# Performance work log

Hardware: AMD Instinct MI355X
Metric: run time of the kernel (lower is better)

## Reference

```python
import jax, jax.numpy as jnp
import numpy as np

N = 50000   # nodes
E = 800000  # edges
G = 64      # graphs
D_IN = 128
D_OUT = 64
HID = 2 * D_OUT  # 128, hidden width of non-final layers
EPS = 1e-5


def _seg_sum(v, idx, n):
    return jax.ops.segment_sum(v, idx, num_segments=n)


def _gcn(x, W, b, src, dst, n):
    # GCNConv with default add_self_loops=True, edge_weight=1, sym norm
    xw = x @ W                                            # [N, out]
    deg = _seg_sum(jnp.ones(src.shape[0], x.dtype), dst, n) + 1.0  # +1 self loop
    dis = jax.lax.rsqrt(deg)                              # deg^{-1/2}, deg>=1
    norm = dis[src] * dis[dst]                            # [E]
    agg = _seg_sum(norm[:, None] * xw[src], dst, n)       # gather-scale-scatter
    return agg + (dis * dis)[:, None] * xw + b            # self-loop term + bias


def _mpnn_layer(x, src, dst, edge_attr, gw, gb, ew, eb, n):
    h = _gcn(x, gw, gb, src, dst, n)
    e = jax.nn.relu(edge_attr[:, None] * ew + eb)         # Linear(1,out).relu per edge
    msg = h[src] + e                                      # message = x_j + edge_attr
    cnt = _seg_sum(jnp.ones(src.shape[0], x.dtype), dst, n)
    return _seg_sum(msg, dst, n) / jnp.clip(cnt, 1.0)[:, None]  # scatter-mean


def _ln(x, g, b):
    # node-wise LayerNorm over feature dim
    mu = x.mean(-1, keepdims=True)
    var = x.var(-1, keepdims=True)
    return (x - mu) * jax.lax.rsqrt(var + EPS) * g + b


def setup_inputs() -> dict:
    key = jax.random.key(0)
    ks = jax.random.split(key, 24)
    x = jax.random.normal(ks[0], (N, D_IN), jnp.float32)
    edge_index = jax.random.randint(ks[1], (2, E), 0, N, dtype=jnp.int64)
    edge_attr = jax.random.uniform(ks[2], (E,), jnp.float32)
    batch = jnp.sort(jax.random.randint(ks[3], (N,), 0, G, dtype=jnp.int64))

    def lin(k, fan_in, shape):
        return jax.random.uniform(k, shape, jnp.float32, -1.0, 1.0) / np.sqrt(fan_in)

    # layer 0: in 128 -> 128; layer 1: 128 -> 128; layer 2: 128 -> 64
    inp = {
        "x": x, "edge_index": edge_index, "edge_attr": edge_attr, "batch": batch,
        "gcn_w0": lin(ks[4], D_IN, (D_IN, HID)),  "gcn_b0": jnp.zeros((HID,), jnp.float32),
        "edge_w0": lin(ks[5], 1, (HID,)),          "edge_b0": lin(ks[6], 1, (HID,)),
        "ln_g0": jnp.ones((HID,), jnp.float32),   "ln_b0": jnp.zeros((HID,), jnp.float32),
        "gcn_w1": lin(ks[7], HID, (HID, HID)),    "gcn_b1": jnp.zeros((HID,), jnp.float32),
        "edge_w1": lin(ks[8], 1, (HID,)),          "edge_b1": lin(ks[9], 1, (HID,)),
        "ln_g1": jnp.ones((HID,), jnp.float32),   "ln_b1": jnp.zeros((HID,), jnp.float32),
        "gcn_w2": lin(ks[10], HID, (HID, D_OUT)), "gcn_b2": jnp.zeros((D_OUT,), jnp.float32),
        "edge_w2": lin(ks[11], 1, (D_OUT,)),       "edge_b2": lin(ks[12], 1, (D_OUT,)),
    }
    return inp


def reference(x, edge_index, edge_attr, batch,
              gcn_w0, gcn_b0, edge_w0, edge_b0, ln_g0, ln_b0,
              gcn_w1, gcn_b1, edge_w1, edge_b1, ln_g1, ln_b1,
              gcn_w2, gcn_b2, edge_w2, edge_b2):
    src, dst = edge_index[0], edge_index[1]
    h = _mpnn_layer(x, src, dst, edge_attr, gcn_w0, gcn_b0, edge_w0, edge_b0, N)
    h = _ln(jax.nn.relu(h), ln_g0, ln_b0)
    h = _mpnn_layer(h, src, dst, edge_attr, gcn_w1, gcn_b1, edge_w1, edge_b1, N)
    h = _ln(jax.nn.relu(h), ln_g1, ln_b1)
    h = _mpnn_layer(h, src, dst, edge_attr, gcn_w2, gcn_b2, edge_w2, edge_b2, N)
    # global_mean_pool
    cnt = _seg_sum(jnp.ones((N,), h.dtype), batch, G)
    z_pooled = _seg_sum(h, batch, G) / jnp.clip(cnt, 1.0)[:, None]
    return h, z_pooled
```

## Files before the change

### kernel.cpp

```cpp
#include <hip/hip_runtime.h>

#define NN 50000
#define NE 800000
#define NG 64
#define HID 128
#define DOUT 64
#define LN_EPS 1e-5f
#define NBUK 391
#define BCAP 3072
#define EPB 8192

typedef unsigned int uint32;
typedef unsigned short ushort16;

__device__ inline ushort16 f2bf(float f) {
  uint32 u = __float_as_uint(f);
  u += 0x7fffu + ((u >> 16) & 1u);
  return (ushort16)(u >> 16);
}
__device__ inline uint32 pack2(float x, float y) {
  return (uint32)f2bf(x) | ((uint32)f2bf(y) << 16);
}
__device__ inline float bflo(uint32 p) { return __uint_as_float(p << 16); }
__device__ inline float bfhi(uint32 p) { return __uint_as_float(p & 0xffff0000u); }

__global__ __launch_bounds__(256) void k_zero_f(float* p, int n) {
  int i = blockIdx.x * 256 + threadIdx.x;
  if (i < n) p[i] = 0.f;
}

__global__ __launch_bounds__(256) void k_init_bcur(int* __restrict__ bcur) {
  int i = blockIdx.x * 256 + threadIdx.x;
  if (i < NBUK) bcur[i] = i * BCAP;
}

__global__ __launch_bounds__(1024) void k_bucket(const int* __restrict__ src,
                                                 const int* __restrict__ dst,
                                                 const float* __restrict__ ea,
                                                 int* __restrict__ bcur,
                                                 uint2* __restrict__ tmp, int e) {
  __shared__ int hist[NBUK], lbase[NBUK], lcur[NBUK];
  int t = threadIdx.x;
  for (int i = t; i < NBUK; i += 1024) {
    hist[i] = 0;
    lcur[i] = 0;
  }
  __syncthreads();
  int base_e = blockIdx.x * EPB;
  int dstv[EPB / 1024];
#pragma unroll
  for (int k = 0; k < EPB / 1024; k++) {
    int i = base_e + k * 1024 + t;
    int d = (i < e) ? dst[i] : -1;
    dstv[k] = d;
    if (d >= 0) atomicAdd(&hist[d >> 7], 1);
  }
  __syncthreads();
  for (int i = t; i < NBUK; i += 1024) {
    int c = hist[i];
    int b = 0;
    if (c > 0) b = atomicAdd(&bcur[i], c);
    lbase[i] = b;
  }
  __syncthreads();
#pragma unroll
  for (int k = 0; k < EPB / 1024; k++) {
    int i = base_e + k * 1024 + t;
    int d = dstv[k];
    if (d >= 0) {
      int b = d >> 7;
      int r = atomicAdd(&lcur[b], 1);
      int pos = lbase[b] + r;
      if (pos < (b + 1) * BCAP) {
        uint2 rec;
        rec.x = (uint32)(src[i] & 0xffff) | ((uint32)(d & 127) << 16);
        rec.y = __float_as_uint(ea[i]);
        tmp[pos] = rec;
      }
    }
  }
}

__global__ __launch_bounds__(512) void k_bscan(const int* __restrict__ bcur,
                                               int* __restrict__ bbase,
                                               int* __restrict__ rowptr) {
  __shared__ int s[512];
  int t = threadIdx.x;
  int v = 0;
  if (t < NBUK) {
    v = bcur[t] - t * BCAP;
    if (v > BCAP) v = BCAP;
  }
  s[t] = v;
  __syncthreads();
  for (int off = 1; off < 512; off <<= 1) {
    int x = (t >= off) ? s[t - off] : 0;
    __syncthreads();
    s[t] += x;
    __syncthreads();
  }
  if (t < NBUK) bbase[t] = s[t] - v;
  if (t == 511) {
    bbase[NBUK] = s[511];
    rowptr[NN] = s[511];
  }
}

__global__ __launch_bounds__(256) void k_bsort(const uint2* __restrict__ tmp,
                                               const int* __restrict__ bcur,
                                               const int* __restrict__ bbase,
                                               int* __restrict__ rowptr,
                                               int* __restrict__ csrc,
                                               float* __restrict__ cea,
                                               float* __restrict__ dis,
                                               float* __restrict__ invc) {
  int b = blockIdx.x;
  __shared__ int hist[128], excl[128], cur[128];
  int t = threadIdx.x;
  if (t < 128) {
    hist[t] = 0;
    cur[t] = 0;
  }
  __syncthreads();
  int cnt = bcur[b] - b * BCAP;
  if (cnt > BCAP) cnt = BCAP;
  int tb = b * BCAP;
  int ob = bbase[b];
  for (int i = t; i < cnt; i += 256) {
    uint2 r = tmp[tb + i];
    atomicAdd(&hist[(r.x >> 16) & 127], 1);
  }
  __syncthreads();
  int myDeg = (t < 128) ? hist[t] : 0;
  for (int off = 1; off < 128; off <<= 1) {
    int x = 0;
    if (t < 128 && t >= off) x = hist[t - off];
    __syncthreads();
    if (t < 128) hist[t] += x;
    __syncthreads();
  }
  if (t < 128) {
    excl[t] = hist[t] - myDeg;
    int node = (b << 7) + t;
    if (node < NN) {
      rowptr[node] = ob + excl[t];
      dis[node] = rsqrtf((float)(myDeg + 1));
      invc[node] = (myDeg > 0) ? 1.0f / (float)myDeg : 1.0f;
    }
  }
  __syncthreads();
  for (int i = t; i < cnt; i += 256) {
    uint2 r = tmp[tb + i];
    int o = (r.x >> 16) & 127;
    int p = atomicAdd(&cur[o], 1);
    int pos = ob + excl[o] + p;
    csrc[pos] = (int)(r.x & 0xffffu);
    cea[pos] = __uint_as_float(r.y);
  }
}

template <int FOUT, bool IN_BF, bool OUT_BF>
__global__ __launch_bounds__(256) void k_gemm(const void* __restrict__ Xv,
                                              const float* __restrict__ W,
                                              void* __restrict__ Yv, int n) {
  const int FI = 128;
  __shared__ __align__(16) float xs[32][FI];
  int t = threadIdx.x;
  int row0 = blockIdx.x * 32;
  if (IN_BF) {
    const ushort16* Xb = (const ushort16*)Xv;
    for (int i = t; i < 32 * 32; i += 256) {
      int r = i >> 5, c = i & 31;
      uint2 v = make_uint2(0u, 0u);
      if (row0 + r < n) v = ((const uint2*)(Xb + (size_t)(row0 + r) * FI))[c];
      float4 f = {bflo(v.x), bfhi(v.x), bflo(v.y), bfhi(v.y)};
      ((float4*)xs[r])[c] = f;
    }
  } else {
    const float* X = (const float*)Xv;
    for (int i = t; i < 32 * FI / 4; i += 256) {
      int r = i / (FI / 4);
      int c = i % (FI / 4);
      float4 v = make_float4(0.f, 0.f, 0.f, 0.f);
      if (row0 + r < n) v = ((const float4*)(X + (size_t)(row0 + r) * FI))[c];
      ((float4*)xs[r])[c] = v;
    }
  }
  __syncthreads();
  const int CG = FOUT / 4;
  const int RG = 256 / CG;
  const int RPT = 32 / RG;
  int cg = t % CG;
  int rg = t / CG;
  float acc[RPT][4];
#pragma unroll
  for (int r = 0; r < RPT; r++)
#pragma unroll
    for (int c = 0; c < 4; c++) acc[r][c] = 0.f;

#pragma unroll 2
  for (int k4 = 0; k4 < FI / 4; k4++) {
    float4 wv[4];
#pragma unroll
    for (int kk = 0; kk < 4; kk++)
      wv[kk] = ((const float4*)(W + (size_t)(4 * k4 + kk) * FOUT))[cg];
#pragma unroll
    for (int r = 0; r < RPT; r++) {
      float4 xv = ((const float4*)xs[rg * RPT + r])[k4];
      acc[r][0] += xv.x * wv[0].x + xv.y * wv[1].x + xv.z * wv[2].x + xv.w * wv[3].x;
      acc[r][1] += xv.x * wv[0].y + xv.y * wv[1].y + xv.z * wv[2].y + xv.w * wv[3].y;
      acc[r][2] += xv.x * wv[0].z + xv.y * wv[1].z + xv.z * wv[2].z + xv.w * wv[3].z;
      acc[r][3] += xv.x * wv[0].w + xv.y * wv[1].w + xv.z * wv[2].w + xv.w * wv[3].w;
    }
  }
#pragma unroll
  for (int r = 0; r < RPT; r++) {
    int row = row0 + rg * RPT + r;
    if (row < n) {
      if (OUT_BF) {
        uint2 o = {pack2(acc[r][0], acc[r][1]), pack2(acc[r][2], acc[r][3])};
        ((uint2*)((ushort16*)Yv + (size_t)row * FOUT))[cg] = o;
      } else {
        float4 o = {acc[r][0], acc[r][1], acc[r][2], acc[r][3]};
        ((float4*)((float*)Yv + (size_t)row * FOUT))[cg] = o;
      }
    }
  }
}

__global__ __launch_bounds__(256) void k_agg_bf(const uint32* __restrict__ XWb,
                                                const float* __restrict__ dis,
                                                const int* __restrict__ rowptr,
                                                const int* __restrict__ csrc,
                                                const float* __restrict__ bias,
                                                uint32* __restrict__ Hb, int n) {
  int lane = threadIdx.x & 63;
  int node = blockIdx.x * 4 + (threadIdx.x >> 6);
  if (node >= n) return;
  float dn = dis[node];
  int beg = rowptr[node], end = rowptr[node + 1];
  float ax = 0.f, ay = 0.f;
  int i = beg;
  for (; i + 4 <= end; i += 4) {
    int s0 = csrc[i], s1 = csrc[i + 1], s2 = csrc[i + 2], s3 = csrc[i + 3];
    float n0 = dn * dis[s0], n1 = dn * dis[s1], n2 = dn * dis[s2], n3 = dn * dis[s3];
    uint32 p0 = XWb[(size_t)s0 * 64 + lane];
    uint32 p1 = XWb[(size_t)s1 * 64 + lane];
    uint32 p2 = XWb[(size_t)s2 * 64 + lane];
    uint32 p3 = XWb[(size_t)s3 * 64 + lane];
    ax += n0 * bflo(p0) + n1 * bflo(p1) + n2 * bflo(p2) + n3 * bflo(p3);
    ay += n0 * bfhi(p0) + n1 * bfhi(p1) + n2 * bfhi(p2) + n3 * bfhi(p3);
  }
  for (; i < end; i++) {
    int s = csrc[i];
    float nr = dn * dis[s];
    uint32 p = XWb[(size_t)s * 64 + lane];
    ax += nr * bflo(p);
    ay += nr * bfhi(p);
  }
  uint32 ps = XWb[(size_t)node * 64 + lane];
  float2 bb = ((const float2*)bias)[lane];
  float d2 = dn * dn;
  float hx = ax + d2 * bflo(ps) + bb.x;
  float hy = ay + d2 * bfhi(ps) + bb.y;
  Hb[(size_t)node * 64 + lane] = pack2(hx, hy);
}

__global__ __launch_bounds__(256) void k_msg_bf(const uint32* __restrict__ Hb,
                                                const float* __restrict__ ew,
                                                const float* __restrict__ eb,
                                                const int* __restrict__ rowptr,
                                                const int* __restrict__ csrc,
                                                const float* __restrict__ cea,
                                                const float* __restrict__ invc,
                                                const float* __restrict__ lng,
                                                const float* __restrict__ lnb,
                                                uint32* __restrict__ OUTb, int n) {
  int lane = threadIdx.x & 63;
  int node = blockIdx.x * 4 + (threadIdx.x >> 6);
  if (node >= n) return;
  int beg = rowptr[node], end = rowptr[node + 1];
  float2 w = ((const float2*)ew)[lane];
  float2 b = ((const float2*)eb)[lane];
  float ax = 0.f, ay = 0.f;
  int i = beg;
  for (; i + 4 <= end; i += 4) {
    int s0 = csrc[i], s1 = csrc[i + 1], s2 = csrc[i + 2], s3 = csrc[i + 3];
    float a0 = cea[i], a1 = cea[i + 1], a2 = cea[i + 2], a3 = cea[i + 3];
    uint32 p0 = Hb[(size_t)s0 * 64 + lane];
    uint32 p1 = Hb[(size_t)s1 * 64 + lane];
    uint32 p2 = Hb[(size_t)s2 * 64 + lane];
    uint32 p3 = Hb[(size_t)s3 * 64 + lane];
    ax += bflo(p0) + fmaxf(a0 * w.x + b.x, 0.f) + bflo(p1) + fmaxf(a1 * w.x + b.x, 0.f) +
          bflo(p2) + fmaxf(a2 * w.x + b.x, 0.f) + bflo(p3) + fmaxf(a3 * w.x + b.x, 0.f);
    ay += bfhi(p0) + fmaxf(a0 * w.y + b.y, 0.f) + bfhi(p1) + fmaxf(a1 * w.y + b.y, 0.f) +
          bfhi(p2) + fmaxf(a2 * w.y + b.y, 0.f) + bfhi(p3) + fmaxf(a3 * w.y + b.y, 0.f);
  }
  for (; i < end; i++) {
    int s = csrc[i];
    float a = cea[i];
    uint32 p = Hb[(size_t)s * 64 + lane];
    ax += bflo(p) + fmaxf(a * w.x + b.x, 0.f);
    ay += bfhi(p) + fmaxf(a * w.y + b.y, 0.f);
  }
  float ic = invc[node];
  float ox = fmaxf(ax * ic, 0.f);
  float oy = fmaxf(ay * ic, 0.f);
  float s1 = ox + oy;
  float s2 = ox * ox + oy * oy;
  for (int off = 32; off; off >>= 1) {
    s1 += __shfl_xor(s1, off, 64);
    s2 += __shfl_xor(s2, off, 64);
  }
  float mu = s1 * (1.f / 128.f);
  float var = s2 * (1.f / 128.f) - mu * mu;
  float r = rsqrtf(var + LN_EPS);
  float2 g = ((const float2*)lng)[lane];
  float2 bb = ((const float2*)lnb)[lane];
  ox = (ox - mu) * r * g.x + bb.x;
  oy = (oy - mu) * r * g.y + bb.y;
  OUTb[(size_t)node * 64 + lane] = pack2(ox, oy);
}

__global__ __launch_bounds__(256) void k_agg64(const float* __restrict__ XW,
                                               const float* __restrict__ dis,
                                               const int* __restrict__ rowptr,
                                               const int* __restrict__ csrc,
                                               const float* __restrict__ bias,
                                               float* __restrict__ H, int n) {
  int lane = threadIdx.x & 63;
  int node = blockIdx.x * 4 + (threadIdx.x >> 6);
  if (node >= n) return;
  float dn = dis[node];
  int beg = rowptr[node], end = rowptr[node + 1];
  float acc = 0.f;
  int i = beg;
  for (; i + 4 <= end; i += 4) {
    int s0 = csrc[i], s1 = csrc[i + 1], s2 = csrc[i + 2], s3 = csrc[i + 3];
    float n0 = dn * dis[s0], n1 = dn * dis[s1], n2 = dn * dis[s2], n3 = dn * dis[s3];
    acc += n0 * XW[(size_t)s0 * 64 + lane] + n1 * XW[(size_t)s1 * 64 + lane] +
           n2 * XW[(size_t)s2 * 64 + lane] + n3 * XW[(size_t)s3 * 64 + lane];
  }
  for (; i < end; i++) {
    int s = csrc[i];
    acc += dn * dis[s] * XW[(size_t)s * 64 + lane];
  }
  float d2 = dn * dn;
  H[(size_t)node * 64 + lane] = acc + d2 * XW[(size_t)node * 64 + lane] + bias[lane];
}

__global__ __launch_bounds__(256) void k_msg64(const float* __restrict__ H,
                                               const float* __restrict__ ew,
                                               const float* __restrict__ eb,
                                               const int* __restrict__ rowptr,
                                               const int* __restrict__ csrc,
                                               const float* __restrict__ cea,
                                               const float* __restrict__ invc,
                                               float* __restrict__ OUT, int n) {
  int lane = threadIdx.x & 63;
  int node = blockIdx.x * 4 + (threadIdx.x >> 6);
  if (node >= n) return;
  int beg = rowptr[node], end = rowptr[node + 1];
  float w = ew[lane], b = eb[lane];
  float acc = 0.f;
  int i = beg;
  for (; i + 4 <= end; i += 4) {
    int s0 = csrc[i], s1 = csrc[i + 1], s2 = csrc[i + 2], s3 = csrc[i + 3];
    float a0 = cea[i], a1 = cea[i + 1], a2 = cea[i + 2], a3 = cea[i + 3];
    acc += H[(size_t)s0 * 64 + lane] + fmaxf(a0 * w + b, 0.f) +
           H[(size_t)s1 * 64 + lane] + fmaxf(a1 * w + b, 0.f) +
           H[(size_t)s2 * 64 + lane] + fmaxf(a2 * w + b, 0.f) +
           H[(size_t)s3 * 64 + lane] + fmaxf(a3 * w + b, 0.f);
  }
  for (; i < end; i++) {
    int s = csrc[i];
    acc += H[(size_t)s * 64 + lane] + fmaxf(cea[i] * w + b, 0.f);
  }
  OUT[(size_t)node * 64 + lane] = acc * invc[node];
}

#define POOL_BLOCKS 256
__global__ __launch_bounds__(256) void k_pool_partial(const float* __restrict__ H,
                                                      const int* __restrict__ batch,
                                                      float* __restrict__ Z, int n) {
  int lane = threadIdx.x & 63;
  int wid = blockIdx.x * 4 + (threadIdx.x >> 6);
  const int WAVES = POOL_BLOCKS * 4;
  int per = (n + WAVES - 1) / WAVES;
  int beg = wid * per;
  int end = beg + per;
  if (end > n) end = n;
  if (beg >= end) return;
  int g = batch[beg];
  float acc = 0.f;
  for (int i = beg; i < end; i++) {
    int gi = batch[i];
    if (gi != g) {
      atomicAdd(&Z[g * 64 + lane], acc);
      acc = 0.f;
      g = gi;
    }
    acc += H[(size_t)i * 64 + lane];
  }
  atomicAdd(&Z[g * 64 + lane], acc);
}

__global__ __launch_bounds__(64) void k_pool_div(float* __restrict__ Z,
                                                 const int* __restrict__ batch, int n) {
  int g = blockIdx.x;
  __shared__ int scnt;
  if (threadIdx.x == 0) {
    int lo = 0, hi = n;
    while (lo < hi) { int m = (lo + hi) >> 1; if (batch[m] < g) lo = m + 1; else hi = m; }
    int b0 = lo;
    lo = 0; hi = n;
    while (lo < hi) { int m = (lo + hi) >> 1; if (batch[m] < g + 1) lo = m + 1; else hi = m; }
    scnt = lo - b0;
  }
  __syncthreads();
  float c = (float)scnt;
  if (c < 1.f) c = 1.f;
  Z[g * 64 + threadIdx.x] /= c;
}

extern "C" void kernel_launch(void* const* d_in, const int* in_sizes, int n_in,
                              void* d_out, int out_size, void* d_ws, size_t ws_size,
                              hipStream_t stream) {
  const float* x = (const float*)d_in[0];
  const int* ei = (const int*)d_in[1];
  const float* ea = (const float*)d_in[2];
  const int* batch = (const int*)d_in[3];
  const float* gw0 = (const float*)d_in[4];
  const float* gb0 = (const float*)d_in[5];
  const float* ew0 = (const float*)d_in[6];
  const float* eb0 = (const float*)d_in[7];
  const float* lg0 = (const float*)d_in[8];
  const float* lb0 = (const float*)d_in[9];
  const float* gw1 = (const float*)d_in[10];
  const float* gb1 = (const float*)d_in[11];
  const float* ew1 = (const float*)d_in[12];
  const float* eb1 = (const float*)d_in[13];
  const float* lg1 = (const float*)d_in[14];
  const float* lb1 = (const float*)d_in[15];
  const float* gw2 = (const float*)d_in[16];
  const float* gb2 = (const float*)d_in[17];
  const float* ew2 = (const float*)d_in[18];
  const float* eb2 = (const float*)d_in[19];
  float* out = (float*)d_out;

  const int* src = ei;
  const int* dst = ei + NE;

  char* w = (char*)d_ws;
  size_t off = 0;
  auto alloc = [&](size_t bytes) -> void* {
    void* p = (void*)(w + off);
    off = (off + bytes + 255) & ~(size_t)255;
    return p;
  };
  int* rowptr = (int*)alloc((NN + 1) * sizeof(int));
  int* bcur = (int*)alloc(NBUK * sizeof(int));
  int* bbase = (int*)alloc((NBUK + 1) * sizeof(int));
  int* csrc = (int*)alloc(NE * sizeof(int));
  float* cea = (float*)alloc(NE * sizeof(float));
  float* dis = (float*)alloc(NN * sizeof(float));
  float* invc = (float*)alloc(NN * sizeof(float));
  uint32* B1b = (uint32*)alloc((size_t)NN * 64 * sizeof(uint32));
  uint32* B2b = (uint32*)alloc((size_t)NN * 64 * sizeof(uint32));
  float* F1 = (float*)alloc((size_t)NN * 64 * sizeof(float));
  float* F2 = (float*)alloc((size_t)NN * 64 * sizeof(float));
  uint2* tmp = (uint2*)F1;

  hipLaunchKernelGGL(k_init_bcur, dim3((NBUK + 255) / 256), dim3(256), 0, stream, bcur);
  hipLaunchKernelGGL(k_bucket, dim3((NE + EPB - 1) / EPB), dim3(1024), 0, stream, src, dst, ea,
                     bcur, tmp, NE);
  hipLaunchKernelGGL(k_bscan, dim3(1), dim3(512), 0, stream, bcur, bbase, rowptr);
  hipLaunchKernelGGL(k_bsort, dim3(NBUK), dim3(256), 0, stream, tmp, bcur, bbase, rowptr, csrc,
                     cea, dis, invc);

  dim3 gemm_grid((NN + 31) / 32), tb(256);
  dim3 node_grid((NN + 3) / 4);

  hipLaunchKernelGGL((k_gemm<128, false, true>), gemm_grid, tb, 0, stream, x, gw0, B1b, NN);
  hipLaunchKernelGGL(k_agg_bf, node_grid, tb, 0, stream, B1b, dis, rowptr, csrc, gb0, B2b, NN);
  hipLaunchKernelGGL(k_msg_bf, node_grid, tb, 0, stream, B2b, ew0, eb0, rowptr, csrc, cea, invc,
                     lg0, lb0, B1b, NN);
  hipLaunchKernelGGL((k_gemm<128, true, true>), gemm_grid, tb, 0, stream, B1b, gw1, B2b, NN);
  hipLaunchKernelGGL(k_agg_bf, node_grid, tb, 0, stream, B2b, dis, rowptr, csrc, gb1, B1b, NN);
  hipLaunchKernelGGL(k_msg_bf, node_grid, tb, 0, stream, B1b, ew1, eb1, rowptr, csrc, cea, invc,
                     lg1, lb1, B2b, NN);
  hipLaunchKernelGGL((k_gemm<64, true, false>), gemm_grid, tb, 0, stream, B2b, gw2, F1, NN);
  hipLaunchKernelGGL(k_agg64, node_grid, tb, 0, stream, F1, dis, rowptr, csrc, gb2, F2, NN);
  hipLaunchKernelGGL(k_msg64, node_grid, tb, 0, stream, F2, ew2, eb2, rowptr, csrc, cea, invc,
                     out, NN);
  float* Z = out + (size_t)NN * 64;
  hipLaunchKernelGGL(k_zero_f, dim3((NG * 64 + 255) / 256), dim3(256), 0, stream, Z, NG * 64);
  hipLaunchKernelGGL(k_pool_partial, dim3(POOL_BLOCKS), tb, 0, stream, out, batch, Z, NN);
  hipLaunchKernelGGL(k_pool_div, dim3(NG), dim3(64), 0, stream, Z, batch, NN);
}
```

Before: 509.0 us.

## Rewrite node GEMM with bf16 MFMA 16x16x32 tiles of 64 rows

Replaces the FP32 scalar FMA GEMM with a matrix-core version. Each block converts W to bf16 into transposed LDS, stages 64 input rows as bf16, and each wave computes a 16-row strip with mfma_f32_16x16x32_bf16. This is meant to cut the ALU cost of the three dense transforms. In exchange, the first layer's fp32 input and all weights are now rounded to bf16, and every block redundantly converts the full weight matrix. Output stores are scalar 2-byte or 4-byte writes rather than vectors.

```diff
diff --git a/kernel.cpp b/kernel.cpp
--- a/kernel.cpp
+++ b/kernel.cpp
@@ -12,6 +12,8 @@
 
 typedef unsigned int uint32;
 typedef unsigned short ushort16;
+typedef __attribute__((ext_vector_type(8))) short bf16x8;
+typedef __attribute__((ext_vector_type(4))) float f32x4;
 
 __device__ inline ushort16 f2bf(float f) {
   uint32 u = __float_as_uint(f);
@@ -163,66 +165,57 @@
 __global__ __launch_bounds__(256) void k_gemm(const void* __restrict__ Xv,
                                               const float* __restrict__ W,
                                               void* __restrict__ Yv, int n) {
-  const int FI = 128;
-  __shared__ __align__(16) float xs[32][FI];
+  const int NT = FOUT / 16;
+  __shared__ __align__(16) unsigned short Wt[FOUT][136];
+  __shared__ __align__(16) unsigned short Xs[64][136];
   int t = threadIdx.x;
-  int row0 = blockIdx.x * 32;
+  int row0 = blockIdx.x * 64;
+  for (int idx = t; idx < 128 * FOUT; idx += 256) {
+    int k = idx / FOUT, col = idx % FOUT;
+    Wt[col][k] = (unsigned short)f2bf(W[idx]);
+  }
   if (IN_BF) {
-    const ushort16* Xb = (const ushort16*)Xv;
-    for (int i = t; i < 32 * 32; i += 256) {
-      int r = i >> 5, c = i & 31;
-      uint2 v = make_uint2(0u, 0u);
-      if (row0 + r < n) v = ((const uint2*)(Xb + (size_t)(row0 + r) * FI))[c];
-      float4 f = {bflo(v.x), bfhi(v.x), bflo(v.y), bfhi(v.y)};
-      ((float4*)xs[r])[c] = f;
+    const uint32* Xb = (const uint32*)Xv;
+    for (int idx = t; idx < 64 * 64; idx += 256) {
+      int r = idx >> 6, c = idx & 63;
+      uint32 v = (row0 + r < n) ? Xb[(size_t)(row0 + r) * 64 + c] : 0u;
+      *(uint32*)&Xs[r][c * 2] = v;
     }
   } else {
-    const float* X = (const float*)Xv;
-    for (int i = t; i < 32 * FI / 4; i += 256) {
-      int r = i / (FI / 4);
-      int c = i % (FI / 4);
-      float4 v = make_float4(0.f, 0.f, 0.f, 0.f);
-      if (row0 + r < n) v = ((const float4*)(X + (size_t)(row0 + r) * FI))[c];
-      ((float4*)xs[r])[c] = v;
-    }
-  }
-  __syncthreads();
-  const int CG = FOUT / 4;
-  const int RG = 256 / CG;
-  const int RPT = 32 / RG;
-  int cg = t % CG;
-  int rg = t / CG;
-  float acc[RPT][4];
-#pragma unroll
-  for (int r = 0; r < RPT; r++)
-#pragma unroll
-    for (int c = 0; c < 4; c++) acc[r][c] = 0.f;
-
-#pragma unroll 2
-  for (int k4 = 0; k4 < FI / 4; k4++) {
-    float4 wv[4];
-#pragma unroll
-    for (int kk = 0; kk < 4; kk++)
-      wv[kk] = ((const float4*)(W + (size_t)(4 * k4 + kk) * FOUT))[cg];
-#pragma unroll
-    for (int r = 0; r < RPT; r++) {
-      float4 xv = ((const float4*)xs[rg * RPT + r])[k4];
-      acc[r][0] += xv.x * wv[0].x + xv.y * wv[1].x + xv.z * wv[2].x + xv.w * wv[3].x;
-      acc[r][1] += xv.x * wv[0].y + xv.y * wv[1].y + xv.z * wv[2].y + xv.w * wv[3].y;
-      acc[r][2] += xv.x * wv[0].z + xv.y * wv[1].z + xv.z * wv[2].z + xv.w * wv[3].z;
-      acc[r][3] += xv.x * wv[0].w + xv.y * wv[1].w + xv.z * wv[2].w + xv.w * wv[3].w;
-    }
-  }
-#pragma unroll
-  for (int r = 0; r < RPT; r++) {
-    int row = row0 + rg * RPT + r;
-    if (row < n) {
-      if (OUT_BF) {
-        uint2 o = {pack2(acc[r][0], acc[r][1]), pack2(acc[r][2], acc[r][3])};
-        ((uint2*)((ushort16*)Yv + (size_t)row * FOUT))[cg] = o;
-      } else {
-        float4 o = {acc[r][0], acc[r][1], acc[r][2], acc[r][3]};
-        ((float4*)((float*)Yv + (size_t)row * FOUT))[cg] = o;
+    const float* Xf = (const float*)Xv;
+    for (int idx = t; idx < 64 * 64; idx += 256) {
+      int r = idx >> 6, c = idx & 63;
+      float2 v = make_float2(0.f, 0.f);
+      if (row0 + r < n) v = ((const float2*)(Xf + (size_t)(row0 + r) * 128))[c];
+      *(uint32*)&Xs[r][c * 2] = pack2(v.x, v.y);
+    }
+  }
+  __syncthreads();
+  int lane = t & 63, wv = t >> 6;
+  int mrow = lane & 15, q = lane >> 4;
+  f32x4 acc[NT];
+#pragma unroll
+  for (int c = 0; c < NT; c++) acc[c] = (f32x4){0.f, 0.f, 0.f, 0.f};
+#pragma unroll
+  for (int kt = 0; kt < 4; kt++) {
+    bf16x8 af = *(const bf16x8*)&Xs[wv * 16 + mrow][kt * 32 + q * 8];
+#pragma unroll
+    for (int c = 0; c < NT; c++) {
+      bf16x8 bfg = *(const bf16x8*)&Wt[c * 16 + mrow][kt * 32 + q * 8];
+      acc[c] = __builtin_amdgcn_mfma_f32_16x16x32_bf16(af, bfg, acc[c], 0, 0, 0);
+    }
+  }
+#pragma unroll
+  for (int c = 0; c < NT; c++) {
+    int cg = c * 16 + mrow;
+#pragma unroll
+    for (int r = 0; r < 4; r++) {
+      int rg = row0 + wv * 16 + q * 4 + r;
+      if (rg < n) {
+        if (OUT_BF)
+          ((unsigned short*)Yv)[(size_t)rg * FOUT + cg] = (unsigned short)f2bf(acc[c][r]);
+        else
+          ((float*)Yv)[(size_t)rg * FOUT + cg] = acc[c][r];
       }
     }
   }
@@ -478,7 +471,7 @@
   hipLaunchKernelGGL(k_bsort, dim3(NBUK), dim3(256), 0, stream, tmp, bcur, bbase, rowptr, csrc,
                      cea, dis, invc);
 
-  dim3 gemm_grid((NN + 31) / 32), tb(256);
+  dim3 gemm_grid((NN + 63) / 64), tb(256);
   dim3 node_grid((NN + 3) / 4);
 
   hipLaunchKernelGGL((k_gemm<128, false, true>), gemm_grid, tb, 0, stream, x, gw0, B1b, NN);
```

After: 462.1 us. 9.2% less time.
